# Kernel optimization log

Hardware: AMD Instinct MI355X
Metric: run time of the kernel (lower is better)

The kernel has to match this reference:

```python
import jax, jax.numpy as jnp
import numpy as np

B, T, F = 16384, 128, 29   # batch, horizon, exogenous features per step
Y_ORDER = 3
K = 512                    # hidden nodes
D_IN = F + Y_ORDER


def setup_inputs() -> dict:
    key = jax.random.key(0)
    ks = jax.random.split(key, 4)
    X = jax.random.normal(ks[0], (B, T, F), dtype=jnp.float32)
    y0 = jax.random.normal(ks[1], (B, Y_ORDER), dtype=jnp.float32)
    # small init scale to keep tanh out of saturation over the long horizon
    W1 = jax.random.normal(ks[2], (D_IN, K), dtype=jnp.float32) * 0.05
    b1 = jnp.zeros((K,), dtype=jnp.float32)
    W2 = jax.random.normal(ks[3], (K, 1), dtype=jnp.float32) * 0.05
    b2 = jnp.zeros((1,), dtype=jnp.float32)
    return {"X": X, "y0": y0, "W1": W1, "b1": b1, "W2": W2, "b2": b2}


def reference(X, y0, W1, b1, W2, b2):
    # State fb: [B, Y_ORDER] where fb[:, i] == feedback_i of the original code
    # (fb[:, 0] is the most recent prediction after the shift).
    def step(fb, x_t):
        # concat order in original: [x, feedback_0, feedback_1, ...]
        inp = jnp.concatenate([x_t, fb], axis=1)            # [B, D_IN]
        h = jnp.tanh(inp @ W1 + b1)                         # [B, K]
        pred = h @ W2 + b2                                  # [B, 1]
        # shift: feedback_i <- feedback_{i-1}; feedback_0 <- pred
        new_fb = jnp.concatenate([pred, fb[:, :-1]], axis=1)
        return new_fb, pred

    X_t = jnp.transpose(X, (1, 0, 2))                       # [T, B, F]
    _, preds = jax.lax.scan(step, y0, X_t)                  # preds: [T, B, 1]
    return jnp.transpose(preds, (1, 0, 2))                  # [B, T, 1]
```

## Files before the change

kernel.cpp:

```cpp
#include <hip/hip_runtime.h>

#define B_TOT 16384
#define T_STEPS 128
#define F_IN 29
#define K_HID 512
#define D_IN 32
#define NW 4
#define NTILE 8
#define XS 33

typedef __attribute__((ext_vector_type(8))) short short8;
typedef __attribute__((ext_vector_type(4))) float floatx4;

__device__ __forceinline__ float fast_tanh(float x) {
    float e = __expf(2.0f * x);
    return 1.0f - 2.0f * __builtin_amdgcn_rcpf(e + 1.0f);
}
__device__ __forceinline__ short bf16_hi_bits(float x) {
    return (short)(__float_as_uint(x) >> 16);
}
__device__ __forceinline__ float bf16_hi_f(float x) {
    return __uint_as_float(__float_as_uint(x) & 0xffff0000u);
}

__global__ __launch_bounds__(256, 2)
void narx_wave4(const float* __restrict__ X,
                const float* __restrict__ y0,
                const float* __restrict__ W1,
                const float* __restrict__ b1,
                const float* __restrict__ W2,
                const float* __restrict__ b2,
                float* __restrict__ out)
{
    __shared__ float sX[2][16 * XS];
    __shared__ float pp[2][NW][16];
    __shared__ short8 sWlo[NW * NTILE * 64];

    const int tid  = threadIdx.x;
    const int wv   = tid >> 6;
    const int lane = tid & 63;
    const int q    = lane >> 4;
    const int m    = lane & 15;
    const size_t row0 = (size_t)blockIdx.x * 16;

    short8 whi[NTILE];
    float b1v[NTILE], w2v[NTILE];
    #pragma unroll
    for (int nt = 0; nt < NTILE; ++nt) {
        int node = wv * (NTILE * 16) + nt * 16 + m;
        short8 lo;
        #pragma unroll
        for (int j = 0; j < 8; ++j) {
            int k = q * 8 + j;
            float v  = W1[k * K_HID + node];
            float hf = bf16_hi_f(v);
            whi[nt][j] = bf16_hi_bits(v);
            lo[j]      = bf16_hi_bits(v - hf);
        }
        sWlo[(wv * NTILE + nt) * 64 + lane] = lo;
        b1v[nt] = b1[node];
        w2v[nt] = W2[node];
    }
    const float b2v = b2[0];
    const short8* wloP = &sWlo[wv * NTILE * 64 + lane];

    float fb0 = y0[(row0 + m) * 3 + 0];
    float fb1 = y0[(row0 + m) * 3 + 1];
    float fb2 = y0[(row0 + m) * 3 + 2];

    const float* Xblk = X + row0 * (T_STEPS * F_IN);
    const int f0 = tid;
    const int f1 = tid + 256;
    const bool v1 = (f1 < 16 * F_IN);
    const int r0 = f0 / F_IN, c0 = f0 - r0 * F_IN;
    const int r1 = f1 / F_IN, c1 = f1 - r1 * F_IN;
    const int xo0 = r0 * (T_STEPS * F_IN) + c0;
    const int xo1 = r1 * (T_STEPS * F_IN) + c1;
    const int lo0 = r0 * XS + c0;
    const int lo1 = r1 * XS + c1;

    float xp0 = Xblk[xo0];
    float xp1 = v1 ? Xblk[xo1] : 0.f;
    sX[0][lo0] = xp0;
    if (v1) sX[0][lo1] = xp1;

    float4 pv = make_float4(0.f, 0.f, 0.f, 0.f);

    for (int t = 0; t < T_STEPS; ++t) {
        const int cur = t & 1;
        __syncthreads();

        if (t > 0) {
            const int pb = cur ^ 1;
            float fbn = pp[pb][0][m] + pp[pb][1][m]
                      + pp[pb][2][m] + pp[pb][3][m] + b2v;
            fb2 = fb1; fb1 = fb0; fb0 = fbn;
            if (wv == 0 && m < 4) {
                const int ro = q * 4 + m;
                float po = pp[pb][0][ro] + pp[pb][1][ro]
                         + pp[pb][2][ro] + pp[pb][3][ro] + b2v;
                pv = make_float4(pv.y, pv.z, pv.w, po);
                if (((t - 1) & 3) == 3)
                    *(float4*)&out[(row0 + ro) * T_STEPS + (t - 4)] = pv;
            }
        }

        const float* sxm = &sX[cur][m * XS];
        short8 ahi, alo;
        #pragma unroll
        for (int j = 0; j < 8; ++j) {
            float xj = sxm[q * 8 + j];
            if (q == 3 && j == 5) xj = fb0;
            if (q == 3 && j == 6) xj = fb1;
            if (q == 3 && j == 7) xj = fb2;
            float hf = bf16_hi_f(xj);
            ahi[j] = bf16_hi_bits(xj);
            alo[j] = bf16_hi_bits(xj - hf);
        }

        const int tn = (t + 1 < T_STEPS) ? (t + 1) : t;
        xp0 = Xblk[xo0 + tn * F_IN];
        if (v1) xp1 = Xblk[xo1 + tn * F_IN];

        float pa0 = 0.f, pa1 = 0.f, pa2 = 0.f, pa3 = 0.f;
        #pragma unroll
        for (int nt = 0; nt < NTILE; ++nt) {
            short8 wl = wloP[nt * 64];
            floatx4 c = {b1v[nt], b1v[nt], b1v[nt], b1v[nt]};
            c = __builtin_amdgcn_mfma_f32_16x16x32_bf16(ahi, whi[nt], c, 0, 0, 0);
            c = __builtin_amdgcn_mfma_f32_16x16x32_bf16(ahi, wl,      c, 0, 0, 0);
            c = __builtin_amdgcn_mfma_f32_16x16x32_bf16(alo, whi[nt], c, 0, 0, 0);
            pa0 = fmaf(fast_tanh(c[0]), w2v[nt], pa0);
            pa1 = fmaf(fast_tanh(c[1]), w2v[nt], pa1);
            pa2 = fmaf(fast_tanh(c[2]), w2v[nt], pa2);
            pa3 = fmaf(fast_tanh(c[3]), w2v[nt], pa3);
        }

        #pragma unroll
        for (int mask = 1; mask <= 8; mask <<= 1) {
            pa0 += __shfl_xor(pa0, mask, 64);
            pa1 += __shfl_xor(pa1, mask, 64);
            pa2 += __shfl_xor(pa2, mask, 64);
            pa3 += __shfl_xor(pa3, mask, 64);
        }

        if (m == 0)
            *(float4*)&pp[cur][wv][q * 4] = make_float4(pa0, pa1, pa2, pa3);

        sX[cur ^ 1][lo0] = xp0;
        if (v1) sX[cur ^ 1][lo1] = xp1;
    }

    __syncthreads();
    if (wv == 0 && m < 4) {
        const int pb = (T_STEPS - 1) & 1;
        const int ro = q * 4 + m;
        float po = pp[pb][0][ro] + pp[pb][1][ro]
                 + pp[pb][2][ro] + pp[pb][3][ro] + b2v;
        pv = make_float4(pv.y, pv.z, pv.w, po);
        *(float4*)&out[(row0 + ro) * T_STEPS + (T_STEPS - 4)] = pv;
    }
}

extern "C" void kernel_launch(void* const* d_in, const int* in_sizes, int n_in,
                              void* d_out, int out_size, void* d_ws, size_t ws_size,
                              hipStream_t stream) {
    const float* X  = (const float*)d_in[0];
    const float* y0 = (const float*)d_in[1];
    const float* W1 = (const float*)d_in[2];
    const float* b1 = (const float*)d_in[3];
    const float* W2 = (const float*)d_in[4];
    const float* b2 = (const float*)d_in[5];
    float* out = (float*)d_out;

    dim3 grid(B_TOT / 16);
    dim3 block(64 * NW);
    narx_wave4<<<grid, block, 0, stream>>>(X, y0, W1, b1, W2, b2, out);
}
```

Before: 640.5 us.

## Split exogenous matmul off the feedback path and add feedback terms via FMAs

Result: slower. 726.0 us (+13.3%).

```diff
diff --git a/kernel.cpp b/kernel.cpp
--- a/kernel.cpp
+++ b/kernel.cpp
@@ -4,33 +4,40 @@
 #define T_STEPS 128
 #define F_IN 29
 #define K_HID 512
-#define D_IN 32
 #define NW 4
 #define NTILE 8
-#define XS 33
+#define XS 29
 
 typedef __attribute__((ext_vector_type(8))) short short8;
 typedef __attribute__((ext_vector_type(4))) float floatx4;
-
-__device__ __forceinline__ float fast_tanh(float x) {
-    float e = __expf(2.0f * x);
-    return 1.0f - 2.0f * __builtin_amdgcn_rcpf(e + 1.0f);
-}
+typedef __attribute__((ext_vector_type(2))) float f32x2;
+
 __device__ __forceinline__ short bf16_hi_bits(float x) {
     return (short)(__float_as_uint(x) >> 16);
 }
 __device__ __forceinline__ float bf16_hi_f(float x) {
     return __uint_as_float(__float_as_uint(x) & 0xffff0000u);
 }
+__device__ __forceinline__ f32x2 tanh2(f32x2 x) {
+    f32x2 a = x + x;
+    f32x2 e;
+    e.x = __expf(a.x);
+    e.y = __expf(a.y);
+    f32x2 d = e + 1.0f;
+    f32x2 r;
+    r.x = __builtin_amdgcn_rcpf(d.x);
+    r.y = __builtin_amdgcn_rcpf(d.y);
+    return 1.0f - 2.0f * r;
+}
 
 __global__ __launch_bounds__(256, 2)
-void narx_wave4(const float* __restrict__ X,
-                const float* __restrict__ y0,
-                const float* __restrict__ W1,
-                const float* __restrict__ b1,
-                const float* __restrict__ W2,
-                const float* __restrict__ b2,
-                float* __restrict__ out)
+void narx_v4(const float* __restrict__ X,
+             const float* __restrict__ y0,
+             const float* __restrict__ W1,
+             const float* __restrict__ b1,
+             const float* __restrict__ W2,
+             const float* __restrict__ b2,
+             float* __restrict__ out)
 {
     __shared__ float sX[2][16 * XS];
     __shared__ float pp[2][NW][16];
@@ -41,48 +48,78 @@
     const int lane = tid & 63;
     const int q    = lane >> 4;
     const int m    = lane & 15;
+    const int q4   = q * 4;
     const size_t row0 = (size_t)blockIdx.x * 16;
 
+    const float* W1r29 = W1 + 29 * K_HID;
+    const float* W1r30 = W1 + 30 * K_HID;
+    const float* W1r31 = W1 + 31 * K_HID;
+    const int nodeBase = wv * (NTILE * 16) + m;
+
     short8 whi[NTILE];
-    float b1v[NTILE], w2v[NTILE];
     #pragma unroll
     for (int nt = 0; nt < NTILE; ++nt) {
-        int node = wv * (NTILE * 16) + nt * 16 + m;
+        int node = nodeBase + nt * 16;
         short8 lo;
         #pragma unroll
         for (int j = 0; j < 8; ++j) {
             int k = q * 8 + j;
-            float v  = W1[k * K_HID + node];
+            float v  = (k < F_IN) ? W1[k * K_HID + node] : 0.f;
             float hf = bf16_hi_f(v);
             whi[nt][j] = bf16_hi_bits(v);
             lo[j]      = bf16_hi_bits(v - hf);
         }
         sWlo[(wv * NTILE + nt) * 64 + lane] = lo;
-        b1v[nt] = b1[node];
-        w2v[nt] = W2[node];
     }
     const float b2v = b2[0];
-    const short8* wloP = &sWlo[wv * NTILE * 64 + lane];
-
-    float fb0 = y0[(row0 + m) * 3 + 0];
-    float fb1 = y0[(row0 + m) * 3 + 1];
-    float fb2 = y0[(row0 + m) * 3 + 2];
+
+    const float* y0r = y0 + (row0 + q4) * 3;
+    float4 fbr0 = make_float4(y0r[0], y0r[3], y0r[6], y0r[9]);
+    float4 fbr1 = make_float4(y0r[1], y0r[4], y0r[7], y0r[10]);
+    float4 fbr2 = make_float4(y0r[2], y0r[5], y0r[8], y0r[11]);
 
     const float* Xblk = X + row0 * (T_STEPS * F_IN);
-    const int f0 = tid;
-    const int f1 = tid + 256;
+    const int f0 = tid, f1 = tid + 256;
     const bool v1 = (f1 < 16 * F_IN);
     const int r0 = f0 / F_IN, c0 = f0 - r0 * F_IN;
     const int r1 = f1 / F_IN, c1 = f1 - r1 * F_IN;
     const int xo0 = r0 * (T_STEPS * F_IN) + c0;
     const int xo1 = r1 * (T_STEPS * F_IN) + c1;
-    const int lo0 = r0 * XS + c0;
-    const int lo1 = r1 * XS + c1;
-
-    float xp0 = Xblk[xo0];
-    float xp1 = v1 ? Xblk[xo1] : 0.f;
-    sX[0][lo0] = xp0;
-    if (v1) sX[0][lo1] = xp1;
+
+    sX[0][f0] = Xblk[xo0];
+    if (v1) sX[0][f1] = Xblk[xo1];
+    sX[1][f0] = Xblk[xo0 + F_IN];
+    if (v1) sX[1][f1] = Xblk[xo1 + F_IN];
+    __syncthreads();
+
+    f32x2 c01[NTILE], c23[NTILE];
+
+    auto compute_base = [&](int buf) {
+        const float* sxm = &sX[buf][m * XS];
+        short8 ahi, alo;
+        #pragma unroll
+        for (int j = 0; j < 8; ++j) {
+            int k = q * 8 + j;
+            float xj = sxm[(k < F_IN) ? k : 0];
+            if (k >= F_IN) xj = 0.f;
+            float hf = bf16_hi_f(xj);
+            ahi[j] = bf16_hi_bits(xj);
+            alo[j] = bf16_hi_bits(xj - hf);
+        }
+        #pragma unroll
+        for (int nt = 0; nt < NTILE; ++nt) {
+            float bb = b1[nodeBase + nt * 16];
+            floatx4 c = {bb, bb, bb, bb};
+            short8 wl = sWlo[(wv * NTILE + nt) * 64 + lane];
+            c = __builtin_amdgcn_mfma_f32_16x16x32_bf16(ahi, whi[nt], c, 0, 0, 0);
+            c = __builtin_amdgcn_mfma_f32_16x16x32_bf16(ahi, wl,      c, 0, 0, 0);
+            c = __builtin_amdgcn_mfma_f32_16x16x32_bf16(alo, whi[nt], c, 0, 0, 0);
+            c01[nt] = (f32x2){c[0], c[1]};
+            c23[nt] = (f32x2){c[2], c[3]};
+        }
+    };
+
+    compute_base(0);
 
     float4 pv = make_float4(0.f, 0.f, 0.f, 0.f);
 
@@ -90,75 +127,83 @@
         const int cur = t & 1;
         __syncthreads();
 
+        float w29t[NTILE], w30t[NTILE], w31t[NTILE], w2t[NTILE];
+        #pragma unroll
+        for (int nt = 0; nt < NTILE; ++nt) {
+            const int no = nodeBase + nt * 16;
+            w29t[nt] = W1r29[no];
+            w30t[nt] = W1r30[no];
+            w31t[nt] = W1r31[no];
+            w2t[nt]  = W2[no];
+        }
+        const int tl = (t + 2 < T_STEPS) ? t + 2 : T_STEPS - 1;
+        float xp0 = Xblk[xo0 + tl * F_IN];
+        float xp1 = v1 ? Xblk[xo1 + tl * F_IN] : 0.f;
+
         if (t > 0) {
             const int pb = cur ^ 1;
-            float fbn = pp[pb][0][m] + pp[pb][1][m]
-                      + pp[pb][2][m] + pp[pb][3][m] + b2v;
-            fb2 = fb1; fb1 = fb0; fb0 = fbn;
+            float4 s0 = *(const float4*)&pp[pb][0][q4];
+            float4 s1 = *(const float4*)&pp[pb][1][q4];
+            float4 s2 = *(const float4*)&pp[pb][2][q4];
+            float4 s3 = *(const float4*)&pp[pb][3][q4];
+            float4 fbn = (s0 + s1) + (s2 + s3);
+            fbn.x += b2v; fbn.y += b2v; fbn.z += b2v; fbn.w += b2v;
+            fbr2 = fbr1; fbr1 = fbr0; fbr0 = fbn;
             if (wv == 0 && m < 4) {
-                const int ro = q * 4 + m;
-                float po = pp[pb][0][ro] + pp[pb][1][ro]
-                         + pp[pb][2][ro] + pp[pb][3][ro] + b2v;
+                float po = m == 0 ? fbn.x : m == 1 ? fbn.y
+                         : m == 2 ? fbn.z : fbn.w;
                 pv = make_float4(pv.y, pv.z, pv.w, po);
                 if (((t - 1) & 3) == 3)
-                    *(float4*)&out[(row0 + ro) * T_STEPS + (t - 4)] = pv;
+                    *(float4*)&out[(row0 + q4 + m) * T_STEPS + (t - 4)] = pv;
             }
         }
 
-        const float* sxm = &sX[cur][m * XS];
-        short8 ahi, alo;
-        #pragma unroll
-        for (int j = 0; j < 8; ++j) {
-            float xj = sxm[q * 8 + j];
-            if (q == 3 && j == 5) xj = fb0;
-            if (q == 3 && j == 6) xj = fb1;
-            if (q == 3 && j == 7) xj = fb2;
-            float hf = bf16_hi_f(xj);
-            ahi[j] = bf16_hi_bits(xj);
-            alo[j] = bf16_hi_bits(xj - hf);
-        }
-
-        const int tn = (t + 1 < T_STEPS) ? (t + 1) : t;
-        xp0 = Xblk[xo0 + tn * F_IN];
-        if (v1) xp1 = Xblk[xo1 + tn * F_IN];
-
-        float pa0 = 0.f, pa1 = 0.f, pa2 = 0.f, pa3 = 0.f;
+        f32x2 fb001 = {fbr0.x, fbr0.y}, fb023 = {fbr0.z, fbr0.w};
+        f32x2 fb101 = {fbr1.x, fbr1.y}, fb123 = {fbr1.z, fbr1.w};
+        f32x2 fb201 = {fbr2.x, fbr2.y}, fb223 = {fbr2.z, fbr2.w};
+        f32x2 pa01 = {0.f, 0.f}, pa23 = {0.f, 0.f};
         #pragma unroll
         for (int nt = 0; nt < NTILE; ++nt) {
-            short8 wl = wloP[nt * 64];
-            floatx4 c = {b1v[nt], b1v[nt], b1v[nt], b1v[nt]};
-            c = __builtin_amdgcn_mfma_f32_16x16x32_bf16(ahi, whi[nt], c, 0, 0, 0);
-            c = __builtin_amdgcn_mfma_f32_16x16x32_bf16(ahi, wl,      c, 0, 0, 0);
-            c = __builtin_amdgcn_mfma_f32_16x16x32_bf16(alo, whi[nt], c, 0, 0, 0);
-            pa0 = fmaf(fast_tanh(c[0]), w2v[nt], pa0);
-            pa1 = fmaf(fast_tanh(c[1]), w2v[nt], pa1);
-            pa2 = fmaf(fast_tanh(c[2]), w2v[nt], pa2);
-            pa3 = fmaf(fast_tanh(c[3]), w2v[nt], pa3);
+            f32x2 h01 = c01[nt] + fb001 * w29t[nt] + fb101 * w30t[nt]
+                                 + fb201 * w31t[nt];
+            f32x2 h23 = c23[nt] + fb023 * w29t[nt] + fb123 * w30t[nt]
+                                 + fb223 * w31t[nt];
+            f32x2 t01 = tanh2(h01);
+            f32x2 t23 = tanh2(h23);
+            pa01 += t01 * w2t[nt];
+            pa23 += t23 * w2t[nt];
         }
 
         #pragma unroll
         for (int mask = 1; mask <= 8; mask <<= 1) {
-            pa0 += __shfl_xor(pa0, mask, 64);
-            pa1 += __shfl_xor(pa1, mask, 64);
-            pa2 += __shfl_xor(pa2, mask, 64);
-            pa3 += __shfl_xor(pa3, mask, 64);
-        }
-
+            pa01.x += __shfl_xor(pa01.x, mask, 64);
+            pa01.y += __shfl_xor(pa01.y, mask, 64);
+            pa23.x += __shfl_xor(pa23.x, mask, 64);
+            pa23.y += __shfl_xor(pa23.y, mask, 64);
+        }
         if (m == 0)
-            *(float4*)&pp[cur][wv][q * 4] = make_float4(pa0, pa1, pa2, pa3);
-
-        sX[cur ^ 1][lo0] = xp0;
-        if (v1) sX[cur ^ 1][lo1] = xp1;
+            *(float4*)&pp[cur][wv][q4] =
+                make_float4(pa01.x, pa01.y, pa23.x, pa23.y);
+
+        sX[cur][f0] = xp0;
+        if (v1) sX[cur][f1] = xp1;
+
+        if (t + 1 < T_STEPS)
+            compute_base(cur ^ 1);
     }
 
     __syncthreads();
     if (wv == 0 && m < 4) {
         const int pb = (T_STEPS - 1) & 1;
-        const int ro = q * 4 + m;
-        float po = pp[pb][0][ro] + pp[pb][1][ro]
-                 + pp[pb][2][ro] + pp[pb][3][ro] + b2v;
+        float4 s0 = *(const float4*)&pp[pb][0][q4];
+        float4 s1 = *(const float4*)&pp[pb][1][q4];
+        float4 s2 = *(const float4*)&pp[pb][2][q4];
+        float4 s3 = *(const float4*)&pp[pb][3][q4];
+        float4 fbn = (s0 + s1) + (s2 + s3);
+        fbn.x += b2v; fbn.y += b2v; fbn.z += b2v; fbn.w += b2v;
+        float po = m == 0 ? fbn.x : m == 1 ? fbn.y : m == 2 ? fbn.z : fbn.w;
         pv = make_float4(pv.y, pv.z, pv.w, po);
-        *(float4*)&out[(row0 + ro) * T_STEPS + (T_STEPS - 4)] = pv;
+        *(float4*)&out[(row0 + q4 + m) * T_STEPS + (T_STEPS - 4)] = pv;
     }
 }
 
@@ -175,5 +220,5 @@
 
     dim3 grid(B_TOT / 16);
     dim3 block(64 * NW);
-    narx_wave4<<<grid, block, 0, stream>>>(X, y0, W1, b1, W2, b2, out);
-}
+    narx_v4<<<grid, block, 0, stream>>>(X, y0, W1, b1, W2, b2, out);
+}
```
